# Optimization experiments

Measured on AMD Instinct MI355X. Metric: run time of the kernel, lower is better.

## Reference

```python
import jax, jax.numpy as jnp
import numpy as np

SR = 16000
HOP = 256
MIN_F0 = 50.0
MAX_F0 = 500.0
MIN_PERIOD = SR // 500          # 32
MAX_PERIOD = SR // 50           # 320
FRAME_LEN = HOP * 2             # 512
LAG_END = min(MAX_PERIOD, FRAME_LEN // 2)  # 256 -> lags 32..255 (224 lags)


def setup_inputs() -> dict:
    key = jax.random.key(0)
    waveform = jax.random.normal(key, (64, 1, 163840), dtype=jnp.float32)
    return {"waveform": waveform}


def reference(waveform):
    B, C, T = waveform.shape
    x = waveform[:, 0, :]  # (B, T)
    pad = FRAME_LEN // 2
    xpad = jnp.pad(x, ((0, 0), (pad, pad)), mode='reflect')
    n_frames = (T + 2 * pad - FRAME_LEN) // HOP + 1  # = T//HOP + 1
    # frame extraction (equivalent to unfold(frame_length, hop))
    idx = np.arange(n_frames)[:, None] * HOP + np.arange(FRAME_LEN)[None, :]
    frames = xpad[:, idx]  # (B, F, L)
    # L2-normalize each frame
    norm = jnp.sqrt(jnp.sum(frames * frames, axis=-1, keepdims=True))
    xn = frames / (norm + 1e-8)
    # zero-pad right so xn[t] * xz[t+p] reproduces frame[:L-p] * frame[p:]
    xz = jnp.pad(xn, ((0, 0), (0, 0), (0, FRAME_LEN)))
    lags = jnp.arange(MIN_PERIOD, LAG_END)

    def step(carry, p):
        sl = jax.lax.dynamic_slice_in_dim(xz, p, FRAME_LEN, axis=-1)
        return carry, jnp.sum(xn * sl, axis=-1)  # (B, F)

    _, ac = jax.lax.scan(step, None, lags)  # (P, B, F)
    max_idx = jnp.argmax(ac, axis=0)  # (B, F)
    period = max_idx.astype(jnp.float32) + MIN_PERIOD
    f0 = SR / (period + 1e-8)
    return jnp.clip(f0, MIN_F0, MAX_F0)  # (B, F)
```

## Files before the change

### kernel.cpp

```cpp
#include <hip/hip_runtime.h>


#define SR_F 16000.0f
#define HOP 256
#define FRAME_LEN 512
#define PAD 256
#define T_LEN 163840
#define N_FRAMES 641
#define TOTAL (64 * N_FRAMES)
#define HALF (TOTAL / 2)
#define MIN_PERIOD 32
#define N_LAGS 224
#define WPB 4
#define NC 15

typedef _Float16 half8 __attribute__((ext_vector_type(8)));
typedef float floatx4 __attribute__((ext_vector_type(4)));
typedef unsigned int uint2v __attribute__((ext_vector_type(2)));

__device__ __forceinline__ int swz(int q) { return q ^ ((q >> 3) & 7); }

__device__ __forceinline__ unsigned int pkh(float a, float b) {
    unsigned short ha = __builtin_bit_cast(unsigned short, (_Float16)a);
    unsigned short hb = __builtin_bit_cast(unsigned short, (_Float16)b);
    return (unsigned int)ha | ((unsigned int)hb << 16);
}

#define DPP_XOR1 0xB1
#define DPP_XOR2 0x4E
#define DPP_ROR4 0x124
#define DPP_ROR8 0x128

template <int CTRL> __device__ __forceinline__ int dppi(int x) {
    return __builtin_amdgcn_update_dpp(0, x, CTRL, 0xF, 0xF, false);
}
template <int CTRL> __device__ __forceinline__ float dppf(float x) {
    return __builtin_bit_cast(float, dppi<CTRL>(__builtin_bit_cast(int, x)));
}

__device__ __forceinline__ uint2v pl16sw(unsigned int x, bool sel) {
#if __has_builtin(__builtin_amdgcn_permlane16_swap)
    (void)sel;
    return __builtin_amdgcn_permlane16_swap(x, x, false, false);
#else
    unsigned int p = (unsigned int)__shfl_xor((int)x, 16);
    uint2v r; r[0] = sel ? p : x; r[1] = sel ? x : p; return r;
#endif
}
__device__ __forceinline__ uint2v pl32sw(unsigned int x, bool sel) {
#if __has_builtin(__builtin_amdgcn_permlane32_swap)
    (void)sel;
    return __builtin_amdgcn_permlane32_swap(x, x, false, false);
#else
    unsigned int p = (unsigned int)__shfl_xor((int)x, 32);
    uint2v r; r[0] = sel ? p : x; r[1] = sel ? x : p; return r;
#endif
}

__device__ __forceinline__ float wave_sum(float x, bool oddrow, bool hihalf) {
    x += dppf<DPP_XOR1>(x);
    x += dppf<DPP_XOR2>(x);
    x += dppf<DPP_ROR4>(x);
    x += dppf<DPP_ROR8>(x);
    uint2v p = pl16sw(__builtin_bit_cast(unsigned int, x), oddrow);
    x = __builtin_bit_cast(float, p[0]) + __builtin_bit_cast(float, p[1]);
    p = pl32sw(__builtin_bit_cast(unsigned int, x), hihalf);
    x = __builtin_bit_cast(float, p[0]) + __builtin_bit_cast(float, p[1]);
    return x;
}

__device__ __forceinline__
void top2_comb(float& v1, int& i1, float& v2, float ov1, int oi1, float ov2) {
    bool take = (ov1 > v1) || (ov1 == v1 && oi1 < i1);
    float lose = take ? v1 : ov1;
    if (take) { v1 = ov1; i1 = oi1; }
    v2 = fmaxf(fmaxf(v2, ov2), lose);
}

template <int CTRL> __device__ __forceinline__
void top2_dpp(float& v1, int& i1, float& v2) {
    float ov1 = dppf<CTRL>(v1);
    int   oi1 = dppi<CTRL>(i1);
    float ov2 = dppf<CTRL>(v2);
    top2_comb(v1, i1, v2, ov1, oi1, ov2);
}

__device__ __forceinline__
void top2_full(floatx4 acc, int qd, int nn, bool oddrow, bool hihalf,
               float& v1, int& i1, float& v2) {
    v1 = acc[0];
    i1 = 64*qd + nn;
    v2 = -__builtin_inff();
    #pragma unroll
    for (int r = 1; r < 4; ++r) {
        float cv = (4*qd + r < 14) ? acc[r] : -__builtin_inff();
        bool take = (cv > v1);
        float lose = take ? v1 : cv;
        if (take) { v1 = cv; i1 = 64*qd + 16*r + nn; }
        v2 = fmaxf(v2, lose);
    }
    top2_dpp<DPP_XOR1>(v1, i1, v2);
    top2_dpp<DPP_XOR2>(v1, i1, v2);
    top2_dpp<DPP_ROR4>(v1, i1, v2);
    top2_dpp<DPP_ROR8>(v1, i1, v2);
    {
        uint2v a = pl16sw(__builtin_bit_cast(unsigned int, v1), oddrow);
        uint2v b = pl16sw((unsigned int)i1, oddrow);
        uint2v c = pl16sw(__builtin_bit_cast(unsigned int, v2), oddrow);
        float ov1 = __builtin_bit_cast(float, oddrow ? a[0] : a[1]);
        int   oi1 = (int)(oddrow ? b[0] : b[1]);
        float ov2 = __builtin_bit_cast(float, oddrow ? c[0] : c[1]);
        top2_comb(v1, i1, v2, ov1, oi1, ov2);
    }
    {
        uint2v a = pl32sw(__builtin_bit_cast(unsigned int, v1), hihalf);
        uint2v b = pl32sw((unsigned int)i1, hihalf);
        uint2v c = pl32sw(__builtin_bit_cast(unsigned int, v2), hihalf);
        float ov1 = __builtin_bit_cast(float, hihalf ? a[0] : a[1]);
        int   oi1 = (int)(hihalf ? b[0] : b[1]);
        float ov2 = __builtin_bit_cast(float, hihalf ? c[0] : c[1]);
        top2_comb(v1, i1, v2, ov1, oi1, ov2);
    }
}

__device__ __forceinline__ void write_copies(unsigned int* e, unsigned int* o,
                                             unsigned int u10, unsigned int u11,
                                             unsigned int u20, unsigned int u21,
                                             int lane) {
    e[120 + 2*lane] = u10;  e[121 + 2*lane] = u11;
    e[248 + 2*lane] = u20;  e[249 + 2*lane] = u21;
    unsigned int a  = __shfl(u10, (lane + 1) & 63);
    unsigned int bb = __shfl(u20, (lane + 1) & 63);
    unsigned int n1 = (lane == 63) ? bb : a;
    unsigned int n2 = (lane == 63) ? 0u : bb;
    o[120 + 2*lane] = (u10 >> 16) | (u11 << 16);
    o[121 + 2*lane] = (u11 >> 16) | (n1 << 16);
    o[248 + 2*lane] = (u20 >> 16) | (u21 << 16);
    o[249 + 2*lane] = (u21 >> 16) | (n2 << 16);
    if (lane == 0) o[119] = u10 << 16;
}

__device__ __forceinline__ void emit(float* out, int bf, int i1) {
    float period = (float)(i1 + MIN_PERIOD);
    float f0 = SR_F / (period + 1e-8f);
    out[bf] = fminf(fmaxf(f0, 50.0f), 500.0f);
}

__device__ __forceinline__ void finish_frame(
    const float* __restrict__ x, int base, bool fast, int bf,
    float* __restrict__ out,
    unsigned int* ye, unsigned int* yo, unsigned int* le, unsigned int* loo,
    float4 c1, float4 c2, floatx4 acc, float qen, int lane,
    int qd, int nn, int par, int wA0, int wB0, int seg,
    bool oddrow, bool hihalf) {

    const unsigned int* ybh = par ? yo : ye;
    const unsigned int* ybl = par ? loo : le;
    const bool s0 = (seg & 1), s1 = (seg & 2), s2 = (seg & 4), s3 = (seg & 8);

    le[lane] = 0u; loo[lane] = 0u;
    if (lane < 56) { le[64 + lane] = 0u; loo[64 + lane] = 0u; }
    if (lane < 25) { le[375 + lane] = 0u; loo[375 + lane] = 0u; }
    if (fast) {
        float l0 = c1.x - (float)(_Float16)c1.x;
        float l1 = c1.y - (float)(_Float16)c1.y;
        float l2 = c1.z - (float)(_Float16)c1.z;
        float l3 = c1.w - (float)(_Float16)c1.w;
        float l4 = c2.x - (float)(_Float16)c2.x;
        float l5 = c2.y - (float)(_Float16)c2.y;
        float l6 = c2.z - (float)(_Float16)c2.z;
        float l7 = c2.w - (float)(_Float16)c2.w;
        write_copies(le, loo, pkh(l0, l1), pkh(l2, l3),
                              pkh(l4, l5), pkh(l6, l7), lane);
    } else {
        for (int t = lane; t < FRAME_LEN; t += 64) {
            int idxr = base + t;
            if (idxr < 0) idxr = -idxr;
            if (idxr >= T_LEN) idxr = 2 * (T_LEN - 1) - idxr;
            float v = x[idxr];
            float l = v - (float)(_Float16)v;
            unsigned short h = __builtin_bit_cast(unsigned short, (_Float16)l);
            ((unsigned short*)le)[240 + t] = h;
            ((unsigned short*)loo)[239 + t] = h;
        }
    }
    __threadfence_block();

    #pragma unroll
    for (int c = 0; c < NC; ++c) {
        uint4 au = *(const uint4*)(ye + (wA0 + 16*c));
        const unsigned int* p = ybl + (wB0 + 16*c);
        uint4 bu; bu.x = p[0]; bu.y = p[1]; bu.z = p[2]; bu.w = p[3];
        acc = __builtin_amdgcn_mfma_f32_16x16x32_f16(
            __builtin_bit_cast(half8, au), __builtin_bit_cast(half8, bu),
            acc, 0, 0, 0);
    }
    #pragma unroll
    for (int c = 0; c < NC; ++c) {
        uint4 au = *(const uint4*)(le + (wA0 + 16*c));
        const unsigned int* p = ybh + (wB0 + 16*c);
        uint4 bu; bu.x = p[0]; bu.y = p[1]; bu.z = p[2]; bu.w = p[3];
        acc = __builtin_amdgcn_mfma_f32_16x16x32_f16(
            __builtin_bit_cast(half8, au), __builtin_bit_cast(half8, bu),
            acc, 0, 0, 0);
    }

    float v1, v2; int i1;
    top2_full(acc, qd, nn, oddrow, hihalf, v1, i1, v2);

    const float E2 = 1.0e-4f * qen + 0.02f;
    if (v1 - v2 > 2.0f * E2) {
        if (lane == 0) emit(out, bf, i1);
        return;
    }

    float* sw = (float*)ye;
    if (fast) {
        const float4* g4 = (const float4*)(x + base);
        ((float4*)sw)[swz(lane)]      = g4[lane];
        ((float4*)sw)[swz(lane + 64)] = g4[lane + 64];
        if (lane < 16) ((float4*)sw)[swz(lane + 128)] = make_float4(0.f,0.f,0.f,0.f);
    } else {
        for (int t = lane; t < FRAME_LEN; t += 64) {
            int idxr = base + t;
            if (idxr < 0) idxr = -idxr;
            if (idxr >= T_LEN) idxr = 2 * (T_LEN - 1) - idxr;
            sw[(swz(t >> 2) << 2) | (t & 3)] = x[idxr];
        }
        int t = FRAME_LEN + lane;
        sw[(swz(t >> 2) << 2) | (t & 3)] = 0.0f;
    }
    __threadfence_block();

    const float4* s4 = (const float4*)sw;
    double dtot[4];
    #pragma unroll
    for (int r = 0; r < 4; ++r) {
        const int g  = (r << 2) + qd;
        const int p0 = MIN_PERIOD + (g << 4);
        double dacc[16];
        #pragma unroll
        for (int j = 0; j < 16; ++j) dacc[j] = 0.0;
        if (g < 14) {
            const int n16 = (FRAME_LEN - p0 + 15) >> 4;
            #pragma unroll
            for (int k = 0; k < 2; ++k) {
                const int ch = seg + (k << 4);
                if (ch < n16) {
                    const int t  = ch << 4;
                    const int qa = t >> 2;
                    const int qw = (t + p0) >> 2;
                    float a[16], w[32];
                    #pragma unroll
                    for (int u = 0; u < 4; ++u) {
                        float4 v = s4[swz(qa + u)];
                        a[4*u+0]=v.x; a[4*u+1]=v.y; a[4*u+2]=v.z; a[4*u+3]=v.w;
                    }
                    #pragma unroll
                    for (int u = 0; u < 8; ++u) {
                        float4 v = s4[swz(qw + u)];
                        w[4*u+0]=v.x; w[4*u+1]=v.y; w[4*u+2]=v.z; w[4*u+3]=v.w;
                    }
                    #pragma unroll
                    for (int j = 0; j < 16; ++j) {
                        #pragma unroll
                        for (int i = 0; i < 16; ++i)
                            dacc[j] = fma((double)a[i], (double)w[i + j], dacc[j]);
                    }
                }
            }
        }
        double u8[8], u4[4], u2[2], dtotal;
        #pragma unroll
        for (int i = 0; i < 8; ++i) {
            double lo = dacc[2*i], hi = dacc[2*i+1];
            double keep = s0 ? hi : lo, send = s0 ? lo : hi;
            u8[i] = keep + __shfl_xor(send, 1);
        }
        #pragma unroll
        for (int i = 0; i < 4; ++i) {
            double lo = u8[2*i], hi = u8[2*i+1];
            double keep = s1 ? hi : lo, send = s1 ? lo : hi;
            u4[i] = keep + __shfl_xor(send, 2);
        }
        #pragma unroll
        for (int i = 0; i < 2; ++i) {
            double lo = u4[2*i], hi = u4[2*i+1];
            double keep = s2 ? hi : lo, send = s2 ? lo : hi;
            u2[i] = keep + __shfl_xor(send, 4);
        }
        {
            double lo = u2[0], hi = u2[1];
            double keep = s3 ? hi : lo, send = s3 ? lo : hi;
            dtotal = keep + __shfl_xor(send, 8);
        }
        dtot[r] = ((r << 6) + lane < N_LAGS) ? dtotal : -__builtin_inf();
    }
    double dv1 = dtot[0];
    int    di1 = lane;
    #pragma unroll
    for (int r = 1; r < 4; ++r) {
        double c = dtot[r];
        if (c > dv1) { dv1 = c; di1 = (r << 6) + lane; }
    }
    #pragma unroll
    for (int m = 1; m < 64; m <<= 1) {
        double o = __shfl_xor(dv1, m);
        int   oi = __shfl_xor(di1, m);
        if (o > dv1 || (o == dv1 && oi < di1)) { dv1 = o; di1 = oi; }
    }
    if (lane == 0) emit(out, bf, di1);
}

__global__ __launch_bounds__(256, 4) void f0_kernel(const float* __restrict__ wav,
                                                    float* __restrict__ out) {
    __shared__ unsigned int yw[WPB][3200];

    const int tid  = threadIdx.x;
    const int wv   = tid >> 6;
    const int lane = tid & 63;
    unsigned int* yeA = yw[wv];
    unsigned int* yoA = yeA + 400;
    unsigned int* leA = yeA + 800;
    unsigned int* loA = yeA + 1200;
    unsigned int* yeB = yeA + 1600;
    unsigned int* yoB = yeA + 2000;
    unsigned int* leB = yeA + 2400;
    unsigned int* loB = yeA + 2800;

    const int xcd = blockIdx.x & 7;
    const int idx = blockIdx.x >> 3;
    const int bfA = (xcd * 641 + idx) * WPB + wv;
    const int bfB = bfA + HALF;
    const int bA  = bfA / N_FRAMES;
    const int fA  = bfA - bA * N_FRAMES;
    const int bB  = bfB / N_FRAMES;
    const int fB  = bfB - bB * N_FRAMES;
    const float* __restrict__ xA = wav + (size_t)bA * T_LEN;
    const float* __restrict__ xB = wav + (size_t)bB * T_LEN;
    const int baseA = fA * HOP - PAD;
    const int baseB = fB * HOP - PAD;
    const bool fastA = (fA != 0 && fA != N_FRAMES - 1);
    const bool fastB = (fB != 0 && fB != N_FRAMES - 1);

    const int qd = lane >> 4;
    const int nn = lane & 15;
    const int par = nn & 1;
    const int wA0 = 120 + 4*qd - 8*nn;
    const int wB0 = 136 + 4*qd + ((nn - par) >> 1);
    const int seg = lane & 15;
    const bool oddrow = (lane & 16) != 0;
    const bool hihalf = (lane & 32) != 0;

    float4 cA1, cA2, cB1, cB2;
    if (fastA) {
        const float4* g4 = (const float4*)(xA + baseA);
        cA1 = g4[lane];
        cA2 = g4[lane + 64];
    }
    if (fastB) {
        const float4* g4 = (const float4*)(xB + baseB);
        cB1 = g4[lane];
        cB2 = g4[lane + 64];
    }
    yeA[lane] = 0u; yoA[lane] = 0u; yeB[lane] = 0u; yoB[lane] = 0u;
    if (lane < 56) { yeA[64+lane]=0u; yoA[64+lane]=0u; yeB[64+lane]=0u; yoB[64+lane]=0u; }
    if (lane < 25) { yeA[375+lane]=0u; yoA[375+lane]=0u; yeB[375+lane]=0u; yoB[375+lane]=0u; }

    float qenA = 0.0f, qenB = 0.0f;
    if (fastA) {
        qenA = cA1.x*cA1.x + cA1.y*cA1.y + cA1.z*cA1.z + cA1.w*cA1.w
             + cA2.x*cA2.x + cA2.y*cA2.y + cA2.z*cA2.z + cA2.w*cA2.w;
        write_copies(yeA, yoA, pkh(cA1.x, cA1.y), pkh(cA1.z, cA1.w),
                               pkh(cA2.x, cA2.y), pkh(cA2.z, cA2.w), lane);
    } else {
        for (int t = lane; t < FRAME_LEN; t += 64) {
            int idxr = baseA + t;
            if (idxr < 0) idxr = -idxr;
            if (idxr >= T_LEN) idxr = 2 * (T_LEN - 1) - idxr;
            float v = xA[idxr];
            qenA = __builtin_fmaf(v, v, qenA);
            unsigned short h = __builtin_bit_cast(unsigned short, (_Float16)v);
            ((unsigned short*)yeA)[240 + t] = h;
            ((unsigned short*)yoA)[239 + t] = h;
        }
    }
    if (fastB) {
        qenB = cB1.x*cB1.x + cB1.y*cB1.y + cB1.z*cB1.z + cB1.w*cB1.w
             + cB2.x*cB2.x + cB2.y*cB2.y + cB2.z*cB2.z + cB2.w*cB2.w;
        write_copies(yeB, yoB, pkh(cB1.x, cB1.y), pkh(cB1.z, cB1.w),
                               pkh(cB2.x, cB2.y), pkh(cB2.z, cB2.w), lane);
    } else {
        for (int t = lane; t < FRAME_LEN; t += 64) {
            int idxr = baseB + t;
            if (idxr < 0) idxr = -idxr;
            if (idxr >= T_LEN) idxr = 2 * (T_LEN - 1) - idxr;
            float v = xB[idxr];
            qenB = __builtin_fmaf(v, v, qenB);
            unsigned short h = __builtin_bit_cast(unsigned short, (_Float16)v);
            ((unsigned short*)yeB)[240 + t] = h;
            ((unsigned short*)yoB)[239 + t] = h;
        }
    }
    __threadfence_block();

    qenA = wave_sum(qenA, oddrow, hihalf);
    qenB = wave_sum(qenB, oddrow, hihalf);

    const unsigned int* ybhA = par ? yoA : yeA;
    const unsigned int* ybhB = par ? yoB : yeB;
    floatx4 aA0 = {0.f,0.f,0.f,0.f}, aA1 = {0.f,0.f,0.f,0.f};
    floatx4 aB0 = {0.f,0.f,0.f,0.f}, aB1 = {0.f,0.f,0.f,0.f};
    #pragma unroll
    for (int c = 0; c < NC; ++c) {
        uint4 auA = *(const uint4*)(yeA + (wA0 + 16*c));
        const unsigned int* pA = ybhA + (wB0 + 16*c);
        uint4 buA; buA.x = pA[0]; buA.y = pA[1]; buA.z = pA[2]; buA.w = pA[3];
        uint4 auB = *(const uint4*)(yeB + (wA0 + 16*c));
        const unsigned int* pB = ybhB + (wB0 + 16*c);
        uint4 buB; buB.x = pB[0]; buB.y = pB[1]; buB.z = pB[2]; buB.w = pB[3];
        if (c & 1) {
            aA1 = __builtin_amdgcn_mfma_f32_16x16x32_f16(
                __builtin_bit_cast(half8, auA), __builtin_bit_cast(half8, buA),
                aA1, 0, 0, 0);
            aB1 = __builtin_amdgcn_mfma_f32_16x16x32_f16(
                __builtin_bit_cast(half8, auB), __builtin_bit_cast(half8, buB),
                aB1, 0, 0, 0);
        } else {
            aA0 = __builtin_amdgcn_mfma_f32_16x16x32_f16(
                __builtin_bit_cast(half8, auA), __builtin_bit_cast(half8, buA),
                aA0, 0, 0, 0);
            aB0 = __builtin_amdgcn_mfma_f32_16x16x32_f16(
                __builtin_bit_cast(half8, auB), __builtin_bit_cast(half8, buB),
                aB0, 0, 0, 0);
        }
    }
    floatx4 accA = aA0 + aA1;
    floatx4 accB = aB0 + aB1;

    float v1A, v2A; int i1A;
    top2_full(accA, qd, nn, oddrow, hihalf, v1A, i1A, v2A);
    float v1B, v2B; int i1B;
    top2_full(accB, qd, nn, oddrow, hihalf, v1B, i1B, v2B);

    const float E1A = 9.765625e-4f * qenA + 0.05f;
    const float E1B = 9.765625e-4f * qenB + 0.05f;
    const bool okA = (v1A - v2A > 2.0f * E1A);
    const bool okB = (v1B - v2B > 2.0f * E1B);

    if (okA) {
        if (lane == 0) emit(out, bfA, i1A);
    }
    if (okB) {
        if (lane == 0) emit(out, bfB, i1B);
    }
    if (!okA)
        finish_frame(xA, baseA, fastA, bfA, out, yeA, yoA, leA, loA,
                     cA1, cA2, accA, qenA, lane, qd, nn, par, wA0, wB0,
                     seg, oddrow, hihalf);
    if (!okB)
        finish_frame(xB, baseB, fastB, bfB, out, yeB, yoB, leB, loB,
                     cB1, cB2, accB, qenB, lane, qd, nn, par, wA0, wB0,
                     seg, oddrow, hihalf);
}

extern "C" void kernel_launch(void* const* d_in, const int* in_sizes, int n_in,
                              void* d_out, int out_size, void* d_ws, size_t ws_size,
                              hipStream_t stream) {
    const float* wav = (const float*)d_in[0];
    float* out = (float*)d_out;
    const int n_blocks = HALF / WPB;
    f0_kernel<<<n_blocks, 256, 0, stream>>>(wav, out);
}
```

Before: 149.1 us.

## Switch to persistent grid of 768 blocks looping over frame pairs per wave

Replaces the one-pair-per-wave launch (5128 blocks) with a fixed grid of 768 blocks where each wave processes 6 or 7 consecutive frame pairs in a loop. The aim is to cut block launch and scheduling overhead and tail imbalance. In exchange, there is no overlap across iterations within a wave, and adjacent pairs assigned to the same wave may give uneven per-wave work when fallback paths trigger. Locality changes because consecutive frames now share a wave.

```diff
diff --git a/kernel.cpp b/kernel.cpp
--- a/kernel.cpp
+++ b/kernel.cpp
@@ -13,6 +13,9 @@
 #define N_LAGS 224
 #define WPB 4
 #define NC 15
+#define NBLK 768
+#define NSLOT (NBLK * WPB)
+#define EXTRA (HALF - 6 * NSLOT)
 
 typedef _Float16 half8 __attribute__((ext_vector_type(8)));
 typedef float floatx4 __attribute__((ext_vector_type(4)));
@@ -328,20 +331,12 @@
     unsigned int* leB = yeA + 2400;
     unsigned int* loB = yeA + 2800;
 
-    const int xcd = blockIdx.x & 7;
-    const int idx = blockIdx.x >> 3;
-    const int bfA = (xcd * 641 + idx) * WPB + wv;
-    const int bfB = bfA + HALF;
-    const int bA  = bfA / N_FRAMES;
-    const int fA  = bfA - bA * N_FRAMES;
-    const int bB  = bfB / N_FRAMES;
-    const int fB  = bfB - bB * N_FRAMES;
-    const float* __restrict__ xA = wav + (size_t)bA * T_LEN;
-    const float* __restrict__ xB = wav + (size_t)bB * T_LEN;
-    const int baseA = fA * HOP - PAD;
-    const int baseB = fB * HOP - PAD;
-    const bool fastA = (fA != 0 && fA != N_FRAMES - 1);
-    const bool fastB = (fB != 0 && fB != N_FRAMES - 1);
+    const int xcd  = blockIdx.x & 7;
+    const int idx  = blockIdx.x >> 3;
+    const int slot = (xcd * (NBLK / 8) + idx) * WPB + wv;
+    int p0, np;
+    if (slot < EXTRA) { p0 = slot * 7;                     np = 7; }
+    else              { p0 = EXTRA * 7 + (slot - EXTRA)*6; np = 6; }
 
     const int qd = lane >> 4;
     const int nn = lane & 15;
@@ -352,116 +347,132 @@
     const bool oddrow = (lane & 16) != 0;
     const bool hihalf = (lane & 32) != 0;
 
-    float4 cA1, cA2, cB1, cB2;
-    if (fastA) {
-        const float4* g4 = (const float4*)(xA + baseA);
-        cA1 = g4[lane];
-        cA2 = g4[lane + 64];
-    }
-    if (fastB) {
-        const float4* g4 = (const float4*)(xB + baseB);
-        cB1 = g4[lane];
-        cB2 = g4[lane + 64];
-    }
-    yeA[lane] = 0u; yoA[lane] = 0u; yeB[lane] = 0u; yoB[lane] = 0u;
-    if (lane < 56) { yeA[64+lane]=0u; yoA[64+lane]=0u; yeB[64+lane]=0u; yoB[64+lane]=0u; }
-    if (lane < 25) { yeA[375+lane]=0u; yoA[375+lane]=0u; yeB[375+lane]=0u; yoB[375+lane]=0u; }
-
-    float qenA = 0.0f, qenB = 0.0f;
-    if (fastA) {
-        qenA = cA1.x*cA1.x + cA1.y*cA1.y + cA1.z*cA1.z + cA1.w*cA1.w
-             + cA2.x*cA2.x + cA2.y*cA2.y + cA2.z*cA2.z + cA2.w*cA2.w;
-        write_copies(yeA, yoA, pkh(cA1.x, cA1.y), pkh(cA1.z, cA1.w),
-                               pkh(cA2.x, cA2.y), pkh(cA2.z, cA2.w), lane);
-    } else {
-        for (int t = lane; t < FRAME_LEN; t += 64) {
-            int idxr = baseA + t;
-            if (idxr < 0) idxr = -idxr;
-            if (idxr >= T_LEN) idxr = 2 * (T_LEN - 1) - idxr;
-            float v = xA[idxr];
-            qenA = __builtin_fmaf(v, v, qenA);
-            unsigned short h = __builtin_bit_cast(unsigned short, (_Float16)v);
-            ((unsigned short*)yeA)[240 + t] = h;
-            ((unsigned short*)yoA)[239 + t] = h;
-        }
-    }
-    if (fastB) {
-        qenB = cB1.x*cB1.x + cB1.y*cB1.y + cB1.z*cB1.z + cB1.w*cB1.w
-             + cB2.x*cB2.x + cB2.y*cB2.y + cB2.z*cB2.z + cB2.w*cB2.w;
-        write_copies(yeB, yoB, pkh(cB1.x, cB1.y), pkh(cB1.z, cB1.w),
-                               pkh(cB2.x, cB2.y), pkh(cB2.z, cB2.w), lane);
-    } else {
-        for (int t = lane; t < FRAME_LEN; t += 64) {
-            int idxr = baseB + t;
-            if (idxr < 0) idxr = -idxr;
-            if (idxr >= T_LEN) idxr = 2 * (T_LEN - 1) - idxr;
-            float v = xB[idxr];
-            qenB = __builtin_fmaf(v, v, qenB);
-            unsigned short h = __builtin_bit_cast(unsigned short, (_Float16)v);
-            ((unsigned short*)yeB)[240 + t] = h;
-            ((unsigned short*)yoB)[239 + t] = h;
-        }
-    }
-    __threadfence_block();
-
-    qenA = wave_sum(qenA, oddrow, hihalf);
-    qenB = wave_sum(qenB, oddrow, hihalf);
-
-    const unsigned int* ybhA = par ? yoA : yeA;
-    const unsigned int* ybhB = par ? yoB : yeB;
-    floatx4 aA0 = {0.f,0.f,0.f,0.f}, aA1 = {0.f,0.f,0.f,0.f};
-    floatx4 aB0 = {0.f,0.f,0.f,0.f}, aB1 = {0.f,0.f,0.f,0.f};
-    #pragma unroll
-    for (int c = 0; c < NC; ++c) {
-        uint4 auA = *(const uint4*)(yeA + (wA0 + 16*c));
-        const unsigned int* pA = ybhA + (wB0 + 16*c);
-        uint4 buA; buA.x = pA[0]; buA.y = pA[1]; buA.z = pA[2]; buA.w = pA[3];
-        uint4 auB = *(const uint4*)(yeB + (wA0 + 16*c));
-        const unsigned int* pB = ybhB + (wB0 + 16*c);
-        uint4 buB; buB.x = pB[0]; buB.y = pB[1]; buB.z = pB[2]; buB.w = pB[3];
-        if (c & 1) {
-            aA1 = __builtin_amdgcn_mfma_f32_16x16x32_f16(
-                __builtin_bit_cast(half8, auA), __builtin_bit_cast(half8, buA),
-                aA1, 0, 0, 0);
-            aB1 = __builtin_amdgcn_mfma_f32_16x16x32_f16(
-                __builtin_bit_cast(half8, auB), __builtin_bit_cast(half8, buB),
-                aB1, 0, 0, 0);
+    for (int t = 0; t < np; ++t) {
+        const int pair = p0 + t;
+        const int bfA = pair;
+        const int bfB = pair + HALF;
+        const int bA  = bfA / N_FRAMES;
+        const int fA  = bfA - bA * N_FRAMES;
+        const int bB  = bfB / N_FRAMES;
+        const int fB  = bfB - bB * N_FRAMES;
+        const float* __restrict__ xA = wav + (size_t)bA * T_LEN;
+        const float* __restrict__ xB = wav + (size_t)bB * T_LEN;
+        const int baseA = fA * HOP - PAD;
+        const int baseB = fB * HOP - PAD;
+        const bool fastA = (fA != 0 && fA != N_FRAMES - 1);
+        const bool fastB = (fB != 0 && fB != N_FRAMES - 1);
+
+        float4 cA1, cA2, cB1, cB2;
+        if (fastA) {
+            const float4* g4 = (const float4*)(xA + baseA);
+            cA1 = g4[lane];
+            cA2 = g4[lane + 64];
+        }
+        if (fastB) {
+            const float4* g4 = (const float4*)(xB + baseB);
+            cB1 = g4[lane];
+            cB2 = g4[lane + 64];
+        }
+        yeA[lane] = 0u; yoA[lane] = 0u; yeB[lane] = 0u; yoB[lane] = 0u;
+        if (lane < 56) { yeA[64+lane]=0u; yoA[64+lane]=0u; yeB[64+lane]=0u; yoB[64+lane]=0u; }
+        if (lane < 25) { yeA[375+lane]=0u; yoA[375+lane]=0u; yeB[375+lane]=0u; yoB[375+lane]=0u; }
+
+        float qenA = 0.0f, qenB = 0.0f;
+        if (fastA) {
+            qenA = cA1.x*cA1.x + cA1.y*cA1.y + cA1.z*cA1.z + cA1.w*cA1.w
+                 + cA2.x*cA2.x + cA2.y*cA2.y + cA2.z*cA2.z + cA2.w*cA2.w;
+            write_copies(yeA, yoA, pkh(cA1.x, cA1.y), pkh(cA1.z, cA1.w),
+                                   pkh(cA2.x, cA2.y), pkh(cA2.z, cA2.w), lane);
         } else {
-            aA0 = __builtin_amdgcn_mfma_f32_16x16x32_f16(
-                __builtin_bit_cast(half8, auA), __builtin_bit_cast(half8, buA),
-                aA0, 0, 0, 0);
-            aB0 = __builtin_amdgcn_mfma_f32_16x16x32_f16(
-                __builtin_bit_cast(half8, auB), __builtin_bit_cast(half8, buB),
-                aB0, 0, 0, 0);
-        }
-    }
-    floatx4 accA = aA0 + aA1;
-    floatx4 accB = aB0 + aB1;
-
-    float v1A, v2A; int i1A;
-    top2_full(accA, qd, nn, oddrow, hihalf, v1A, i1A, v2A);
-    float v1B, v2B; int i1B;
-    top2_full(accB, qd, nn, oddrow, hihalf, v1B, i1B, v2B);
-
-    const float E1A = 9.765625e-4f * qenA + 0.05f;
-    const float E1B = 9.765625e-4f * qenB + 0.05f;
-    const bool okA = (v1A - v2A > 2.0f * E1A);
-    const bool okB = (v1B - v2B > 2.0f * E1B);
-
-    if (okA) {
-        if (lane == 0) emit(out, bfA, i1A);
-    }
-    if (okB) {
-        if (lane == 0) emit(out, bfB, i1B);
-    }
-    if (!okA)
-        finish_frame(xA, baseA, fastA, bfA, out, yeA, yoA, leA, loA,
-                     cA1, cA2, accA, qenA, lane, qd, nn, par, wA0, wB0,
-                     seg, oddrow, hihalf);
-    if (!okB)
-        finish_frame(xB, baseB, fastB, bfB, out, yeB, yoB, leB, loB,
-                     cB1, cB2, accB, qenB, lane, qd, nn, par, wA0, wB0,
-                     seg, oddrow, hihalf);
+            for (int u = lane; u < FRAME_LEN; u += 64) {
+                int idxr = baseA + u;
+                if (idxr < 0) idxr = -idxr;
+                if (idxr >= T_LEN) idxr = 2 * (T_LEN - 1) - idxr;
+                float v = xA[idxr];
+                qenA = __builtin_fmaf(v, v, qenA);
+                unsigned short h = __builtin_bit_cast(unsigned short, (_Float16)v);
+                ((unsigned short*)yeA)[240 + u] = h;
+                ((unsigned short*)yoA)[239 + u] = h;
+            }
+        }
+        if (fastB) {
+            qenB = cB1.x*cB1.x + cB1.y*cB1.y + cB1.z*cB1.z + cB1.w*cB1.w
+                 + cB2.x*cB2.x + cB2.y*cB2.y + cB2.z*cB2.z + cB2.w*cB2.w;
+            write_copies(yeB, yoB, pkh(cB1.x, cB1.y), pkh(cB1.z, cB1.w),
+                                   pkh(cB2.x, cB2.y), pkh(cB2.z, cB2.w), lane);
+        } else {
+            for (int u = lane; u < FRAME_LEN; u += 64) {
+                int idxr = baseB + u;
+                if (idxr < 0) idxr = -idxr;
+                if (idxr >= T_LEN) idxr = 2 * (T_LEN - 1) - idxr;
+                float v = xB[idxr];
+                qenB = __builtin_fmaf(v, v, qenB);
+                unsigned short h = __builtin_bit_cast(unsigned short, (_Float16)v);
+                ((unsigned short*)yeB)[240 + u] = h;
+                ((unsigned short*)yoB)[239 + u] = h;
+            }
+        }
+        __threadfence_block();
+
+        qenA = wave_sum(qenA, oddrow, hihalf);
+        qenB = wave_sum(qenB, oddrow, hihalf);
+
+        const unsigned int* ybhA = par ? yoA : yeA;
+        const unsigned int* ybhB = par ? yoB : yeB;
+        floatx4 aA0 = {0.f,0.f,0.f,0.f}, aA1 = {0.f,0.f,0.f,0.f};
+        floatx4 aB0 = {0.f,0.f,0.f,0.f}, aB1 = {0.f,0.f,0.f,0.f};
+        #pragma unroll
+        for (int c = 0; c < NC; ++c) {
+            uint4 auA = *(const uint4*)(yeA + (wA0 + 16*c));
+            const unsigned int* pA = ybhA + (wB0 + 16*c);
+            uint4 buA; buA.x = pA[0]; buA.y = pA[1]; buA.z = pA[2]; buA.w = pA[3];
+            uint4 auB = *(const uint4*)(yeB + (wA0 + 16*c));
+            const unsigned int* pB = ybhB + (wB0 + 16*c);
+            uint4 buB; buB.x = pB[0]; buB.y = pB[1]; buB.z = pB[2]; buB.w = pB[3];
+            if (c & 1) {
+                aA1 = __builtin_amdgcn_mfma_f32_16x16x32_f16(
+                    __builtin_bit_cast(half8, auA), __builtin_bit_cast(half8, buA),
+                    aA1, 0, 0, 0);
+                aB1 = __builtin_amdgcn_mfma_f32_16x16x32_f16(
+                    __builtin_bit_cast(half8, auB), __builtin_bit_cast(half8, buB),
+                    aB1, 0, 0, 0);
+            } else {
+                aA0 = __builtin_amdgcn_mfma_f32_16x16x32_f16(
+                    __builtin_bit_cast(half8, auA), __builtin_bit_cast(half8, buA),
+                    aA0, 0, 0, 0);
+                aB0 = __builtin_amdgcn_mfma_f32_16x16x32_f16(
+                    __builtin_bit_cast(half8, auB), __builtin_bit_cast(half8, buB),
+                    aB0, 0, 0, 0);
+            }
+        }
+        floatx4 accA = aA0 + aA1;
+        floatx4 accB = aB0 + aB1;
+
+        float v1A, v2A; int i1A;
+        top2_full(accA, qd, nn, oddrow, hihalf, v1A, i1A, v2A);
+        float v1B, v2B; int i1B;
+        top2_full(accB, qd, nn, oddrow, hihalf, v1B, i1B, v2B);
+
+        const float E1A = 9.765625e-4f * qenA + 0.05f;
+        const float E1B = 9.765625e-4f * qenB + 0.05f;
+        const bool okA = (v1A - v2A > 2.0f * E1A);
+        const bool okB = (v1B - v2B > 2.0f * E1B);
+
+        if (okA) {
+            if (lane == 0) emit(out, bfA, i1A);
+        }
+        if (okB) {
+            if (lane == 0) emit(out, bfB, i1B);
+        }
+        if (!okA)
+            finish_frame(xA, baseA, fastA, bfA, out, yeA, yoA, leA, loA,
+                         cA1, cA2, accA, qenA, lane, qd, nn, par, wA0, wB0,
+                         seg, oddrow, hihalf);
+        if (!okB)
+            finish_frame(xB, baseB, fastB, bfB, out, yeB, yoB, leB, loB,
+                         cB1, cB2, accB, qenB, lane, qd, nn, par, wA0, wB0,
+                         seg, oddrow, hihalf);
+    }
 }
 
 extern "C" void kernel_launch(void* const* d_in, const int* in_sizes, int n_in,
@@ -469,6 +480,5 @@
                               hipStream_t stream) {
     const float* wav = (const float*)d_in[0];
     float* out = (float*)d_out;
-    const int n_blocks = HALF / WPB;
-    f0_kernel<<<n_blocks, 256, 0, stream>>>(wav, out);
-}
+    f0_kernel<<<NBLK, 256, 0, stream>>>(wav, out);
+}
```

Result: slower. 190.4 us (+27.7%).
